# Kernel optimization log

Hardware: AMD Instinct MI355X
Metric: run time of the kernel (lower is better)

The kernel has to match this reference:

```python
import jax, jax.numpy as jnp
import numpy as np

NUM_EXPERTS = 8
TOP_K = 2
HIDDEN_DIM = 4096
NUM_TOKENS = 16384


def setup_inputs() -> dict:
    key = jax.random.key(0)
    k1, k2 = jax.random.split(key)
    hidden_states = jax.random.normal(k1, (NUM_TOKENS, HIDDEN_DIM), dtype=jnp.float32)
    # gate weight as in nn.Linear: [num_experts, hidden_dim], init std=0.02
    gate_weight = 0.02 * jax.random.normal(k2, (NUM_EXPERTS, HIDDEN_DIM), dtype=jnp.float32)
    return {"hidden_states": hidden_states, "gate_weight": gate_weight}


def reference(hidden_states, gate_weight):
    # [T, E] router logits (eval mode: no jitter since jitter_noise=0)
    router_logits = jnp.einsum("td,ed->te", hidden_states, gate_weight)
    router_probs = jax.nn.softmax(router_logits.astype(jnp.float32), axis=-1)
    # top-k selection and renormalization
    router_weights, expert_indices = jax.lax.top_k(router_probs, TOP_K)  # [T,K]
    router_weights = router_weights / jnp.sum(router_weights, axis=-1, keepdims=True)
    # load-balance aux loss: E * sum_i f_i * P_i
    num_tokens = router_probs.shape[0]
    expert_mask = jax.nn.one_hot(expert_indices, NUM_EXPERTS, dtype=jnp.float32)  # [T,K,E]
    tokens_per_expert = jnp.sum(expert_mask, axis=(0, 1))  # [E]
    f_i = tokens_per_expert / num_tokens
    p_i = jnp.mean(router_probs, axis=0)
    aux_loss = NUM_EXPERTS * jnp.dot(f_i, p_i)
    return router_weights, expert_indices, aux_loss
```

## Files before the change

kernel.cpp:

```cpp
#include <hip/hip_runtime.h>
#include <math.h>

#define NUM_TOKENS 16384
#define HD 4096
#define HD4 (HD / 4)
#define NE 8
#define TOPK 2

#define BLOCK_THREADS 1024
#define WAVES_PER_BLOCK 16
#define TOK_PER_WAVE 4
#define TOK_PER_BLOCK (WAVES_PER_BLOCK * TOK_PER_WAVE)
#define NUM_BLOCKS (NUM_TOKENS / TOK_PER_BLOCK)
#define KITERS (HD4 / 64)

typedef float vfloat4 __attribute__((ext_vector_type(4)));

__global__ __launch_bounds__(BLOCK_THREADS, 1)
void router_kernel(const float* __restrict__ hidden,
                   const float* __restrict__ gate,
                   float* __restrict__ out_w,
                   float* __restrict__ out_idx,
                   float* __restrict__ accum)
{
    __shared__ vfloat4 g_lds[NE * HD4];
    __shared__ float   s_acc[16];

    const int tid = threadIdx.x;

    const vfloat4* g4 = (const vfloat4*)gate;
    #pragma unroll
    for (int i = 0; i < (NE * HD4) / BLOCK_THREADS; ++i)
        g_lds[tid + i * BLOCK_THREADS] = g4[tid + i * BLOCK_THREADS];
    if (tid < 16) s_acc[tid] = 0.0f;
    __syncthreads();

    const int wave = tid >> 6;
    const int lane = tid & 63;
    const int tokBase = (blockIdx.x * WAVES_PER_BLOCK + wave) * TOK_PER_WAVE;

    const vfloat4* h4 = (const vfloat4*)hidden;
    const size_t rowBase = (size_t)tokBase * HD4 + lane;

    float acc[TOK_PER_WAVE][NE];
    #pragma unroll
    for (int t = 0; t < TOK_PER_WAVE; ++t)
        #pragma unroll
        for (int e = 0; e < NE; ++e) acc[t][e] = 0.0f;

    vfloat4 hbuf[TOK_PER_WAVE];
    #pragma unroll
    for (int t = 0; t < TOK_PER_WAVE; ++t)
        hbuf[t] = __builtin_nontemporal_load(&h4[rowBase + (size_t)t * HD4]);

    #pragma unroll 1
    for (int k = 0; k < KITERS; ++k) {
        vfloat4 hcur[TOK_PER_WAVE];
        #pragma unroll
        for (int t = 0; t < TOK_PER_WAVE; ++t) hcur[t] = hbuf[t];

        if (k + 1 < KITERS) {
            const size_t off = rowBase + (size_t)(k + 1) * 64;
            #pragma unroll
            for (int t = 0; t < TOK_PER_WAVE; ++t)
                hbuf[t] = __builtin_nontemporal_load(&h4[off + (size_t)t * HD4]);
        }

        const int d4 = lane + k * 64;
        #pragma unroll
        for (int e = 0; e < NE; ++e) {
            const vfloat4 g = g_lds[e * HD4 + d4];
            #pragma unroll
            for (int t = 0; t < TOK_PER_WAVE; ++t)
                acc[t][e] += hcur[t].x * g.x + hcur[t].y * g.y
                           + hcur[t].z * g.z + hcur[t].w * g.w;
        }
    }

    #pragma unroll
    for (int t = 0; t < TOK_PER_WAVE; ++t)
        #pragma unroll
        for (int e = 0; e < NE; ++e) {
            float v = acc[t][e];
            #pragma unroll
            for (int off = 32; off >= 1; off >>= 1)
                v += __shfl_xor(v, off, 64);
            acc[t][e] = v;
        }

    if (lane < TOK_PER_WAVE) {
        const int tok = tokBase + lane;
        float p[NE];
        float m = acc[lane][0];
        #pragma unroll
        for (int e = 1; e < NE; ++e) m = fmaxf(m, acc[lane][e]);
        float s = 0.0f;
        #pragma unroll
        for (int e = 0; e < NE; ++e) { p[e] = expf(acc[lane][e] - m); s += p[e]; }
        const float inv = 1.0f / s;
        #pragma unroll
        for (int e = 0; e < NE; ++e) p[e] *= inv;

        int i1 = 0;
        #pragma unroll
        for (int e = 1; e < NE; ++e) if (p[e] > p[i1]) i1 = e;
        int i2 = (i1 == 0) ? 1 : 0;
        #pragma unroll
        for (int e = 0; e < NE; ++e) if (e != i1 && p[e] > p[i2]) i2 = e;

        const float w1 = p[i1], w2 = p[i2];
        const float rs = 1.0f / (w1 + w2);
        out_w[tok * 2 + 0]   = w1 * rs;
        out_w[tok * 2 + 1]   = w2 * rs;
        out_idx[tok * 2 + 0] = (float)i1;
        out_idx[tok * 2 + 1] = (float)i2;

        atomicAdd(&s_acc[i1], 1.0f);
        atomicAdd(&s_acc[i2], 1.0f);
        #pragma unroll
        for (int e = 0; e < NE; ++e) atomicAdd(&s_acc[8 + e], p[e]);
    }
    __syncthreads();
    if (tid < 16) atomicAdd(&accum[tid], s_acc[tid]);
}

__global__ void finalize_kernel(const float* __restrict__ accum,
                                float* __restrict__ aux_out)
{
    if (threadIdx.x == 0) {
        const float invT = 1.0f / (float)NUM_TOKENS;
        float s = 0.0f;
        #pragma unroll
        for (int e = 0; e < NE; ++e)
            s += (accum[e] * invT) * (accum[8 + e] * invT);
        aux_out[0] = (float)NE * s;
    }
}

extern "C" void kernel_launch(void* const* d_in, const int* in_sizes, int n_in,
                              void* d_out, int out_size, void* d_ws, size_t ws_size,
                              hipStream_t stream) {
    const float* hidden = (const float*)d_in[0];
    const float* gate   = (const float*)d_in[1];
    float* out = (float*)d_out;
    float* out_w   = out;
    float* out_idx = out + NUM_TOKENS * 2;
    float* aux     = out + NUM_TOKENS * 4;
    float* accum   = (float*)d_ws;

    (void)hipMemsetAsync(accum, 0, 16 * sizeof(float), stream);
    router_kernel<<<NUM_BLOCKS, BLOCK_THREADS, 0, stream>>>(hidden, gate, out_w, out_idx, accum);
    finalize_kernel<<<1, 64, 0, stream>>>(accum, aux);
}
```

Before: 350.4 us.

## Deepen hidden-state prefetch to four buffers and replace global atomics with per-block partials

```diff
diff --git a/kernel.cpp b/kernel.cpp
--- a/kernel.cpp
+++ b/kernel.cpp
@@ -5,7 +5,6 @@
 #define HD 4096
 #define HD4 (HD / 4)
 #define NE 8
-#define TOPK 2
 
 #define BLOCK_THREADS 1024
 #define WAVES_PER_BLOCK 16
@@ -21,7 +20,7 @@
                    const float* __restrict__ gate,
                    float* __restrict__ out_w,
                    float* __restrict__ out_idx,
-                   float* __restrict__ accum)
+                   float* __restrict__ partial)
 {
     __shared__ vfloat4 g_lds[NE * HD4];
     __shared__ float   s_acc[16];
@@ -48,34 +47,48 @@
         #pragma unroll
         for (int e = 0; e < NE; ++e) acc[t][e] = 0.0f;
 
-    vfloat4 hbuf[TOK_PER_WAVE];
-    #pragma unroll
-    for (int t = 0; t < TOK_PER_WAVE; ++t)
-        hbuf[t] = __builtin_nontemporal_load(&h4[rowBase + (size_t)t * HD4]);
+    vfloat4 bufA[TOK_PER_WAVE], bufB[TOK_PER_WAVE];
+    vfloat4 bufC[TOK_PER_WAVE], bufD[TOK_PER_WAVE];
+
+#define LOADBUF(BUF, KK)                                                     \
+    {                                                                        \
+        const size_t _o = rowBase + (size_t)(KK) * 64;                       \
+        _Pragma("unroll")                                                    \
+        for (int t = 0; t < TOK_PER_WAVE; ++t)                               \
+            BUF[t] = __builtin_nontemporal_load(&h4[_o + (size_t)t * HD4]); \
+    }
+
+#define PHASE(BUF, KK)                                                       \
+    {                                                                        \
+        const int _d4 = lane + (KK) * 64;                                    \
+        _Pragma("unroll")                                                    \
+        for (int e = 0; e < NE; ++e) {                                       \
+            const vfloat4 g = g_lds[e * HD4 + _d4];                          \
+            _Pragma("unroll")                                                \
+            for (int t = 0; t < TOK_PER_WAVE; ++t)                           \
+                acc[t][e] += BUF[t].x * g.x + BUF[t].y * g.y                 \
+                           + BUF[t].z * g.z + BUF[t].w * g.w;                \
+        }                                                                    \
+    }
+
+    LOADBUF(bufA, 0)
+    LOADBUF(bufB, 1)
+    LOADBUF(bufC, 2)
+    LOADBUF(bufD, 3)
 
     #pragma unroll 1
-    for (int k = 0; k < KITERS; ++k) {
-        vfloat4 hcur[TOK_PER_WAVE];
-        #pragma unroll
-        for (int t = 0; t < TOK_PER_WAVE; ++t) hcur[t] = hbuf[t];
-
-        if (k + 1 < KITERS) {
-            const size_t off = rowBase + (size_t)(k + 1) * 64;
-            #pragma unroll
-            for (int t = 0; t < TOK_PER_WAVE; ++t)
-                hbuf[t] = __builtin_nontemporal_load(&h4[off + (size_t)t * HD4]);
-        }
-
-        const int d4 = lane + k * 64;
-        #pragma unroll
-        for (int e = 0; e < NE; ++e) {
-            const vfloat4 g = g_lds[e * HD4 + d4];
-            #pragma unroll
-            for (int t = 0; t < TOK_PER_WAVE; ++t)
-                acc[t][e] += hcur[t].x * g.x + hcur[t].y * g.y
-                           + hcur[t].z * g.z + hcur[t].w * g.w;
-        }
+    for (int k = 0; k < KITERS; k += 4) {
+        PHASE(bufA, k)
+        if (k + 4 < KITERS) LOADBUF(bufA, k + 4)
+        PHASE(bufB, k + 1)
+        if (k + 5 < KITERS) LOADBUF(bufB, k + 5)
+        PHASE(bufC, k + 2)
+        if (k + 6 < KITERS) LOADBUF(bufC, k + 6)
+        PHASE(bufD, k + 3)
+        if (k + 7 < KITERS) LOADBUF(bufD, k + 7)
     }
+#undef LOADBUF
+#undef PHASE
 
     #pragma unroll
     for (int t = 0; t < TOK_PER_WAVE; ++t)
@@ -110,10 +123,10 @@
 
         const float w1 = p[i1], w2 = p[i2];
         const float rs = 1.0f / (w1 + w2);
-        out_w[tok * 2 + 0]   = w1 * rs;
-        out_w[tok * 2 + 1]   = w2 * rs;
-        out_idx[tok * 2 + 0] = (float)i1;
-        out_idx[tok * 2 + 1] = (float)i2;
+        float2 wv = make_float2(w1 * rs, w2 * rs);
+        float2 iv = make_float2((float)i1, (float)i2);
+        *(float2*)&out_w[tok * 2]   = wv;
+        *(float2*)&out_idx[tok * 2] = iv;
 
         atomicAdd(&s_acc[i1], 1.0f);
         atomicAdd(&s_acc[i2], 1.0f);
@@ -121,18 +134,42 @@
         for (int e = 0; e < NE; ++e) atomicAdd(&s_acc[8 + e], p[e]);
     }
     __syncthreads();
-    if (tid < 16) atomicAdd(&accum[tid], s_acc[tid]);
+    if (tid < 16) partial[blockIdx.x * 16 + tid] = s_acc[tid];
 }
 
-__global__ void finalize_kernel(const float* __restrict__ accum,
+__global__ void finalize_kernel(const float* __restrict__ partial,
                                 float* __restrict__ aux_out)
 {
-    if (threadIdx.x == 0) {
+    __shared__ float s_acc[16];
+    const int tid = threadIdx.x;
+    if (tid < 16) s_acc[tid] = 0.0f;
+    __syncthreads();
+
+    float p[16];
+    const vfloat4* p4 = (const vfloat4*)(partial + (size_t)tid * 16);
+    #pragma unroll
+    for (int i = 0; i < 4; ++i) {
+        vfloat4 v = p4[i];
+        p[4 * i + 0] = v.x; p[4 * i + 1] = v.y;
+        p[4 * i + 2] = v.z; p[4 * i + 3] = v.w;
+    }
+    #pragma unroll
+    for (int j = 0; j < 16; ++j) {
+        #pragma unroll
+        for (int off = 32; off >= 1; off >>= 1)
+            p[j] += __shfl_xor(p[j], off, 64);
+    }
+    if ((tid & 63) == 0) {
+        #pragma unroll
+        for (int j = 0; j < 16; ++j) atomicAdd(&s_acc[j], p[j]);
+    }
+    __syncthreads();
+    if (tid == 0) {
         const float invT = 1.0f / (float)NUM_TOKENS;
         float s = 0.0f;
         #pragma unroll
         for (int e = 0; e < NE; ++e)
-            s += (accum[e] * invT) * (accum[8 + e] * invT);
+            s += (s_acc[e] * invT) * (s_acc[8 + e] * invT);
         aux_out[0] = (float)NE * s;
     }
 }
@@ -146,9 +183,8 @@
     float* out_w   = out;
     float* out_idx = out + NUM_TOKENS * 2;
     float* aux     = out + NUM_TOKENS * 4;
-    float* accum   = (float*)d_ws;
+    float* partial = (float*)d_ws;
 
-    (void)hipMemsetAsync(accum, 0, 16 * sizeof(float), stream);
-    router_kernel<<<NUM_BLOCKS, BLOCK_THREADS, 0, stream>>>(hidden, gate, out_w, out_idx, accum);
-    finalize_kernel<<<1, 64, 0, stream>>>(accum, aux);
+    router_kernel<<<NUM_BLOCKS, BLOCK_THREADS, 0, stream>>>(hidden, gate, out_w, out_idx, partial);
+    finalize_kernel<<<1, 256, 0, stream>>>(partial, aux);
 }
```

Result: slower. 629.1 us (+79.5%).
